# Kernel tuning notes

Measured on AMD Instinct MI355X. Metric: run time of the kernel, lower is better.

The kernel has to match this reference:

```python
import jax, jax.numpy as jnp
import numpy as np

D_H = 768
HEAD = 12
D_ATTN = D_H // HEAD


def setup_inputs() -> dict:
    key = jax.random.key(0)
    ks = jax.random.split(key, 9)
    bz, slen = 2, 4096
    scale = 1.0 / np.sqrt(D_H)
    return {
        "v": jax.random.normal(ks[0], (bz, slen, D_H), jnp.float32),
        "k": jax.random.normal(ks[1], (bz, slen, D_H), jnp.float32),
        "q": jax.random.normal(ks[2], (bz, slen, D_H), jnp.float32),
        "mask": jax.random.randint(ks[3], (bz, 1, 1, slen), 0, 2, jnp.int32),
        "w_v": jax.random.normal(ks[4], (D_H, D_H), jnp.float32) * scale,
        "w_k": jax.random.normal(ks[5], (D_H, D_H), jnp.float32) * scale,
        "w_q": jax.random.normal(ks[6], (D_H, D_H), jnp.float32) * scale,
        "w_o": jax.random.normal(ks[7], (D_H, D_H), jnp.float32) * scale,
        "b_o": jax.random.normal(ks[8], (D_H,), jnp.float32) * 0.02,
    }


def _split_head(x, seq_len):
    # (bz, len, d_h) -> (bz, head, len, d_attn)
    bz = x.shape[0]
    return x.reshape(bz, seq_len, HEAD, D_ATTN).transpose(0, 2, 1, 3)


def reference(v, k, q, mask, w_v, w_k, w_q, w_o, b_o):
    len_k, len_q = k.shape[1], q.shape[1]
    vh = _split_head(v @ w_v, len_k)   # (bz, head, len_k, d_attn)
    kh = _split_head(k @ w_k, len_k)
    qh = _split_head(q @ w_q, len_q)
    # scaled dot-product attention with additive mask
    weight = jnp.einsum("bhqd,bhkd->bhqk", qh, kh) / jnp.sqrt(
        jnp.asarray(D_ATTN, jnp.float32)
    )
    weight = weight + mask.astype(weight.dtype) * (-1e9)
    scale_weight = jax.nn.softmax(weight, axis=-1)
    attn = jnp.einsum("bhqk,bhkd->bhqd", scale_weight, vh)
    attn = attn.transpose(0, 2, 1, 3).reshape(-1, len_q, D_H)
    return attn @ w_o + b_o
```

## Files before the change

### kernel.cpp

```cpp
#include <hip/hip_runtime.h>
#include <hip/hip_bf16.h>

#define SLEN 4096
#define DH 768
#define NHEAD 12
#define DA 64

using short8 = __attribute__((ext_vector_type(8))) short;
using f32x4  = __attribute__((ext_vector_type(4))) float;
typedef unsigned uv2 __attribute__((ext_vector_type(2)));

static __device__ __forceinline__ unsigned short f2b(float f) {
    union { __hip_bfloat16 h; unsigned short u; } c;
    c.h = __float2bfloat16(f);
    return c.u;
}

static __device__ __forceinline__ unsigned pkbf(float a, float b) {
    __hip_bfloat162 h = __float22bfloat162_rn(float2{a, b});
    union { __hip_bfloat162 h; unsigned u; } c; c.h = h; return c.u;
}

static __device__ __forceinline__ float fexp2(float x) {
    float r; asm("v_exp_f32 %0, %1" : "=v"(r) : "v"(x)); return r;
}

static __device__ __forceinline__ void swap32(unsigned& a, unsigned& b, int g1) {
#if __has_builtin(__builtin_amdgcn_permlane32_swap)
    uv2 r = __builtin_amdgcn_permlane32_swap(a, b, false, false);
    a = r.x; b = r.y;
#else
    unsigned own = g1 ? b : a, send = g1 ? a : b;
    unsigned recv = __shfl_xor(send, 32);
    unsigned nlo = g1 ? recv : own;
    unsigned nhi = g1 ? own : recv;
    a = nlo; b = nhi;
#endif
}

static __device__ __forceinline__ void swap16(unsigned& a, unsigned& b, int g0) {
#if __has_builtin(__builtin_amdgcn_permlane16_swap)
    uv2 r = __builtin_amdgcn_permlane16_swap(a, b, false, false);
    a = r.x; b = r.y;
#else
    unsigned own = g0 ? b : a, send = g0 ? a : b;
    unsigned recv = __shfl_xor(send, 16);
    unsigned nlo = g0 ? recv : own;
    unsigned nhi = g0 ? own : recv;
    a = nlo; b = nhi;
#endif
}

#define GLD_LDS16(gp, lp) __builtin_amdgcn_global_load_lds( \
    (const __attribute__((address_space(1))) unsigned int*)(gp), \
    (__attribute__((address_space(3))) unsigned int*)(lp), 16, 0, 0)

#define CSCALE 0.18033688011f
#define BIASSTRIDE 4352

__global__ __launch_bounds__(256) void wtrans4(const float* __restrict__ w_v, const float* __restrict__ w_k,
                                               const float* __restrict__ w_q, const float* __restrict__ w_o,
                                               unsigned short* __restrict__ WtV, unsigned short* __restrict__ WtK,
                                               unsigned short* __restrict__ WtQ, unsigned short* __restrict__ WtO,
                                               const int* __restrict__ mask, int* __restrict__ idx,
                                               float* __restrict__ biasC, int* __restrict__ nktArr) {
    const int z = blockIdx.y;
    const int t = threadIdx.x;
    if (z == 4) {
        if (blockIdx.x >= 2) return;
        __shared__ int psum[256];
        const int b = blockIdx.x;
        const int s0 = t * 16;
        const int* mb = mask + b * SLEN;
        int keep[16]; int cnt = 0;
#pragma unroll
        for (int j = 0; j < 16; ++j) { keep[j] = (mb[s0 + j] == 0); cnt += keep[j]; }
        psum[t] = cnt;
        __syncthreads();
        for (int off = 1; off < 256; off <<= 1) {
            int v = psum[t];
            int u = (t >= off) ? psum[t - off] : 0;
            __syncthreads();
            psum[t] = v + u;
            __syncthreads();
        }
        int excl = psum[t] - cnt;
        int total = psum[255];
        int* ib = idx + b * SLEN;
#pragma unroll
        for (int j = 0; j < 16; ++j)
            if (keep[j]) ib[excl++] = s0 + j;
        for (int j = total + t; j < SLEN; j += 256) ib[j] = 0;
        int nkt = (total + 63) >> 6;
        if (nkt < 2) nkt = 2;
        if (t == 0) { nktArr[b] = nkt; nktArr[2 + b] = total; }
        float* bb = biasC + b * BIASSTRIDE;
        for (int j = t; j < BIASSTRIDE; j += 256) bb[j] = (j < total) ? 0.f : -1.442695041e9f;
        return;
    }
    const float* W = (z == 0) ? w_v : (z == 1) ? w_k : (z == 2) ? w_q : w_o;
    unsigned short* Wt = (z == 0) ? WtV : (z == 1) ? WtK : (z == 2) ? WtQ : WtO;
    __shared__ float tile[64][65];
    const int tk = blockIdx.x / 12, tn = blockIdx.x % 12;
    const int k0 = tk * 64, n0 = tn * 64;
#pragma unroll
    for (int i = 0; i < 4; ++i) {
        int uid = t + 256 * i;
        int r = uid >> 4, c = (uid & 15) * 4;
        float4 v4 = *reinterpret_cast<const float4*>(W + (size_t)(k0 + r) * DH + n0 + c);
        tile[r][c] = v4.x; tile[r][c + 1] = v4.y; tile[r][c + 2] = v4.z; tile[r][c + 3] = v4.w;
    }
    __syncthreads();
#pragma unroll
    for (int i = 0; i < 2; ++i) {
        int uid = t + 256 * i;
        int n = uid >> 3, c = (uid & 7) * 8;
        union { unsigned short us[8]; uint4 u; } pk;
#pragma unroll
        for (int j = 0; j < 8; ++j) pk.us[j] = f2b(tile[c + j][n]);
        *reinterpret_cast<uint4*>(Wt + (size_t)(n0 + n) * DH + k0 + c) = pk.u;
    }
}

__global__ __launch_bounds__(256, 3) void proj3(const float* __restrict__ vin, const float* __restrict__ kin,
                                                const float* __restrict__ qin,
                                                const unsigned short* __restrict__ WtV,
                                                const unsigned short* __restrict__ WtK,
                                                const unsigned short* __restrict__ WtQ,
                                                unsigned short* __restrict__ VhTc,
                                                unsigned short* __restrict__ Khc,
                                                unsigned short* __restrict__ Qh,
                                                const int* __restrict__ idx,
                                                const int* __restrict__ nktArr) {
    __shared__ __align__(16) char smem[49152];
    const int t = threadIdx.x;
    const int w = t >> 6, lane = t & 63, lr = lane & 15, lg = lane >> 4;
    const int zz = blockIdx.y;
    const int z = zz / 6, panel = zz % 6;
    const float* X = (z == 0) ? vin : (z == 1) ? kin : qin;
    const unsigned short* Wt = (z == 0) ? WtV : (z == 1) ? WtK : WtQ;
    const int b = blockIdx.x >> 5;
    const int r128 = (blockIdx.x & 31) * 128;
    const bool gather = (z != 2);
    if (gather && r128 >= nktArr[b] * 64) return;
    const int n0 = panel * 128;

    const float* ap[4];
#pragma unroll
    for (int g = 0; g < 4; ++g) {
        int row = w * 32 + g * 8 + (lane >> 3);
        int grow = b * SLEN + (gather ? idx[b * SLEN + r128 + row] : (r128 + row));
        int cj = (lane & 7) ^ (row & 7);
        ap[g] = X + (size_t)grow * DH + cj * 4;
    }
    const unsigned short* bp2[2];
#pragma unroll
    for (int g = 0; g < 2; ++g) {
        int n = w * 32 + g * 16 + (lane >> 2);
        int cj = (lane & 3) ^ (n & 3);
        bp2[g] = Wt + (size_t)(n0 + n) * DH + cj * 8;
    }

    const int arow = w * 32 + lr;
    const int lr7 = lr & 7, lr3 = lr & 3;

    f32x4 acc[2][8] = {};

#define STAGE(PAR) do {                                                              \
        char* ab_ = smem + (PAR) * 16384 + w * 4096;                                 \
        char* bb_ = smem + 32768 + (PAR) * 8192 + w * 2048;                          \
        GLD_LDS16(ap[0], ab_);         GLD_LDS16(ap[1], ab_ + 1024);                 \
        GLD_LDS16(ap[2], ab_ + 2048);  GLD_LDS16(ap[3], ab_ + 3072);                 \
        GLD_LDS16(bp2[0], bb_);        GLD_LDS16(bp2[1], bb_ + 1024);                \
        ap[0] += 32; ap[1] += 32; ap[2] += 32; ap[3] += 32;                          \
        bp2[0] += 32; bp2[1] += 32;                                                  \
    } while (0)

    STAGE(0);
    __syncthreads();

    for (int kt = 0; kt < 24; ++kt) {
        const int par = kt & 1;
        if (kt < 23) STAGE(par ^ 1);
        const char* bufA = smem + par * 16384;
        const char* bufB = smem + 32768 + par * 8192;
        short8 af[2];
#pragma unroll
        for (int mi = 0; mi < 2; ++mi) {
            int r = arow + mi * 16;
            f32x4 alo = *reinterpret_cast<const f32x4*>(bufA + r * 128 + ((2 * lg) ^ lr7) * 16);
            f32x4 ahi = *reinterpret_cast<const f32x4*>(bufA + r * 128 + ((2 * lg + 1) ^ lr7) * 16);
            union { unsigned u[4]; short8 s; } pk;
            pk.u[0] = pkbf(alo[0], alo[1]);
            pk.u[1] = pkbf(alo[2], alo[3]);
            pk.u[2] = pkbf(ahi[0], ahi[1]);
            pk.u[3] = pkbf(ahi[2], ahi[3]);
            af[mi] = pk.s;
        }
        __builtin_amdgcn_s_setprio(1);
#pragma unroll
        for (int ni = 0; ni < 8; ++ni) {
            int n = ni * 16 + lr;
            short8 bf = *reinterpret_cast<const short8*>(bufB + n * 64 + (lg ^ lr3) * 16);
            acc[0][ni] = __builtin_amdgcn_mfma_f32_16x16x32_bf16(af[0], bf, acc[0][ni], 0, 0, 0);
            acc[1][ni] = __builtin_amdgcn_mfma_f32_16x16x32_bf16(af[1], bf, acc[1][ni], 0, 0, 0);
        }
        __builtin_amdgcn_s_setprio(0);
        __syncthreads();
    }
#undef STAGE

    if (z == 0) {
        unsigned short (*tile)[136] = reinterpret_cast<unsigned short(*)[136]>(smem);
#pragma unroll
        for (int mi = 0; mi < 2; ++mi)
#pragma unroll
            for (int ni = 0; ni < 8; ++ni) {
                int n = ni * 16 + lr;
                int j = w * 32 + mi * 16 + lg * 4;
                *reinterpret_cast<unsigned*>(&tile[n][j])     = pkbf(acc[mi][ni][0], acc[mi][ni][1]);
                *reinterpret_cast<unsigned*>(&tile[n][j + 2]) = pkbf(acc[mi][ni][2], acc[mi][ni][3]);
            }
        __syncthreads();
        int n = t >> 1, jc = (t & 1) * 64;
        unsigned short* dst = VhTc +
            ((size_t)(b * NHEAD + 2 * panel + (n >> 6)) * DA + (n & 63)) * SLEN + r128 + jc;
#pragma unroll
        for (int c = 0; c < 8; ++c)
            *reinterpret_cast<uint4*>(dst + c * 8) = *reinterpret_cast<const uint4*>(&tile[n][jc + c * 8]);
    } else {
        unsigned short* Y = (z == 1) ? Khc : Qh;
        const float scale = (z == 2) ? CSCALE : 1.0f;
#pragma unroll
        for (int mi = 0; mi < 2; ++mi)
#pragma unroll
            for (int ni = 0; ni < 8; ++ni) {
                int n = n0 + ni * 16 + lr;
                int h = n >> 6, d = n & 63;
#pragma unroll
                for (int r = 0; r < 4; ++r) {
                    int s = r128 + w * 32 + mi * 16 + lg * 4 + r;
                    Y[(size_t)((b * NHEAD + h) * SLEN + s) * DA + d] = f2b(acc[mi][ni][r] * scale);
                }
            }
    }
}

__global__ __launch_bounds__(256, 3) void attn_kernel(const unsigned short* __restrict__ Qh,
                                                      const unsigned short* __restrict__ Kh,
                                                      const unsigned short* __restrict__ VhT,
                                                      const float* __restrict__ biasC,
                                                      const int* __restrict__ nktArr,
                                                      unsigned short* __restrict__ AT) {
    __shared__ __align__(16) char smem[49152];
    const int t = threadIdx.x;
    const int w = t >> 6, lane = t & 63, lr = lane & 15, lg = lane >> 4;
    const int g0 = (lane >> 4) & 1, g1 = (lane >> 5) & 1;
    const int lr7 = lr & 7;

    const int i = blockIdx.x;
    const int bh = (i & 7) * 3 + ((i >> 3) >> 5);
    const int qb = (i >> 3) & 31;
    const int b = bh / NHEAD;
    const int q0 = qb * 128;
    const size_t base = (size_t)bh * SLEN * DA;
    const int wq0 = q0 + w * 32;
    const int nkt = nktArr[b];
    const int padStart = nktArr[2 + b] >> 6;

    short8 qf[2][2];
#pragma unroll
    for (int mi = 0; mi < 2; ++mi)
#pragma unroll
        for (int ks = 0; ks < 2; ++ks)
            qf[mi][ks] = *reinterpret_cast<const short8*>(
                Qh + base + (size_t)(wq0 + mi * 16 + lr) * DA + ks * 32 + lg * 8);

    const int uid0 = (w << 6) | lane;
    const int r0 = uid0 >> 3;
    const int sc0 = ((uid0 & 7) ^ (r0 & 7)) * 8;
    const unsigned short* kp = Kh + base + (size_t)r0 * DA + sc0;
    const unsigned short* vp = VhT + ((size_t)bh * DA + r0) * SLEN + sc0;
    const float* biasB = biasC + b * BIASSTRIDE + lg * 4;

    const int a0 = lr * 128 + ((lg) ^ lr7) * 16;
    const int a1 = lr * 128 + ((4 + lg) ^ lr7) * 16;

    f32x4 st[2][4];
    f32x4 oacc[2][4] = {};
    f32x4 oacc_l[2] = {};
    f32x4 bias_c[4] = {};
    short8 pa[2][2];
    union { unsigned u[4]; short8 s; } ones;
    ones.u[0] = 0x3F803F80u; ones.u[1] = 0x3F803F80u; ones.u[2] = 0x3F803F80u; ones.u[3] = 0x3F803F80u;

#define STAGE(CB) do {                                                   \
        GLD_LDS16(kp,              smem + (CB) + w * 1024);              \
        GLD_LDS16(kp + 2048,       smem + (CB) + (4 + w) * 1024);        \
        GLD_LDS16(vp,              smem + (CB) + 8192 + w * 1024);       \
        GLD_LDS16(vp + 32 * SLEN,  smem + (CB) + 8192 + (4 + w) * 1024); \
        kp += 64 * DA; vp += 64;                                         \
    } while (0)

#define BIASCOND(TT) do {                                                        \
        if ((TT) >= padStart) {                                                  \
            const float* bpp_ = biasB + (TT) * 64;                               \
            _Pragma("unroll") for (int ni = 0; ni < 4; ++ni)                     \
                bias_c[ni] = *reinterpret_cast<const f32x4*>(bpp_ + ni * 16);    \
        }                                                                        \
    } while (0)

#define QKT(NB) do {                                                                           \
        _Pragma("unroll") for (int ni = 0; ni < 4; ++ni) {                                     \
            short8 kf0 = *reinterpret_cast<const short8*>(smem + (NB) + ni * 2048 + a0);       \
            short8 kf1 = *reinterpret_cast<const short8*>(smem + (NB) + ni * 2048 + a1);       \
            st[0][ni] = __builtin_amdgcn_mfma_f32_16x16x32_bf16(kf1, qf[0][1],                 \
                        __builtin_amdgcn_mfma_f32_16x16x32_bf16(kf0, qf[0][0], bias_c[ni], 0, 0, 0), 0, 0, 0); \
            st[1][ni] = __builtin_amdgcn_mfma_f32_16x16x32_bf16(kf1, qf[1][1],                 \
                        __builtin_amdgcn_mfma_f32_16x16x32_bf16(kf0, qf[1][0], bias_c[ni], 0, 0, 0), 0, 0, 0); \
        }                                                                                      \
    } while (0)

#define PV(CB) do {                                                                                  \
        _Pragma("unroll") for (int ni = 0; ni < 4; ++ni) {                                           \
            short8 vf0 = *reinterpret_cast<const short8*>(smem + (CB) + 8192 + ni * 2048 + a0);      \
            short8 vf1 = *reinterpret_cast<const short8*>(smem + (CB) + 8192 + ni * 2048 + a1);      \
            oacc[0][ni] = __builtin_amdgcn_mfma_f32_16x16x32_bf16(vf0, pa[0][0], oacc[0][ni], 0, 0, 0); \
            oacc[0][ni] = __builtin_amdgcn_mfma_f32_16x16x32_bf16(vf1, pa[0][1], oacc[0][ni], 0, 0, 0); \
            oacc[1][ni] = __builtin_amdgcn_mfma_f32_16x16x32_bf16(vf0, pa[1][0], oacc[1][ni], 0, 0, 0); \
            oacc[1][ni] = __builtin_amdgcn_mfma_f32_16x16x32_bf16(vf1, pa[1][1], oacc[1][ni], 0, 0, 0); \
        }                                                                                            \
        oacc_l[0] = __builtin_amdgcn_mfma_f32_16x16x32_bf16(ones.s, pa[0][0], oacc_l[0], 0, 0, 0);   \
        oacc_l[0] = __builtin_amdgcn_mfma_f32_16x16x32_bf16(ones.s, pa[0][1], oacc_l[0], 0, 0, 0);   \
        oacc_l[1] = __builtin_amdgcn_mfma_f32_16x16x32_bf16(ones.s, pa[1][0], oacc_l[1], 0, 0, 0);   \
        oacc_l[1] = __builtin_amdgcn_mfma_f32_16x16x32_bf16(ones.s, pa[1][1], oacc_l[1], 0, 0, 0);   \
    } while (0)

#define SOFTMAX do {                                                                               \
        _Pragma("unroll") for (int mi = 0; mi < 2; ++mi) {                                         \
            unsigned D[8];                                                                         \
            _Pragma("unroll") for (int ni = 0; ni < 4; ++ni) {                                     \
                float p0 = fexp2(st[mi][ni][0]);                                                   \
                float p1 = fexp2(st[mi][ni][1]);                                                   \
                float p2 = fexp2(st[mi][ni][2]);                                                   \
                float p3 = fexp2(st[mi][ni][3]);                                                   \
                D[ni * 2] = pkbf(p0, p1);                                                          \
                D[ni * 2 + 1] = pkbf(p2, p3);                                                      \
            }                                                                                      \
            swap32(D[0], D[2], g1); swap32(D[1], D[3], g1);                                        \
            swap32(D[4], D[6], g1); swap32(D[5], D[7], g1);                                        \
            swap16(D[0], D[2], g0); swap16(D[1], D[3], g0);                                        \
            swap16(D[4], D[6], g0); swap16(D[5], D[7], g0);                                        \
            union { unsigned u[4]; short8 s; } c0, c1;                                             \
            c0.u[0] = D[0]; c0.u[1] = D[1]; c0.u[2] = D[2]; c0.u[3] = D[3];                        \
            c1.u[0] = D[4]; c1.u[1] = D[5]; c1.u[2] = D[6]; c1.u[3] = D[7];                        \
            pa[mi][0] = c0.s; pa[mi][1] = c1.s;                                                    \
        }                                                                                          \
    } while (0)

#define BODY(KT, CB, NB, NNB) do {                                       \
        SOFTMAX;                                                         \
        __syncthreads();                                                 \
        if ((KT) < nkt - 2) STAGE(NNB);                                  \
        BIASCOND((KT) + 1);                                              \
        __builtin_amdgcn_s_setprio(1);                                   \
        QKT(NB);                                                         \
        PV(CB);                                                          \
        __builtin_amdgcn_s_setprio(0);                                   \
    } while (0)

    STAGE(0);
    __syncthreads();
    STAGE(16384);
    BIASCOND(0);
    __builtin_amdgcn_s_setprio(1);
    QKT(0);
    __builtin_amdgcn_s_setprio(0);

    int kt = 0;
    while (kt + 3 <= nkt - 1) {
        BODY(kt,     0,     16384, 32768);
        BODY(kt + 1, 16384, 32768, 0);
        BODY(kt + 2, 32768, 0,     16384);
        kt += 3;
    }
    const int rem = (nkt - 1) - kt;
    if (rem >= 1) BODY(kt,     0,     16384, 32768);
    if (rem >= 2) BODY(kt + 1, 16384, 32768, 0);
    SOFTMAX;
    {
        const int cbF = ((nkt - 1) % 3) * 16384;
        __builtin_amdgcn_s_setprio(1);
        PV(cbF);
        __builtin_amdgcn_s_setprio(0);
    }

#undef BODY
#undef SOFTMAX
#undef PV
#undef QKT
#undef BIASCOND
#undef STAGE

    {
        __syncthreads();
        float inv[2];
        inv[0] = 1.0f / oacc_l[0][0];
        inv[1] = 1.0f / oacc_l[1][0];
        unsigned* Obw = reinterpret_cast<unsigned*>(smem) + w * (32 * 36);
#pragma unroll
        for (int mi = 0; mi < 2; ++mi)
#pragma unroll
            for (int ni = 0; ni < 4; ++ni) {
                uint2 pr;
                pr.x = pkbf(oacc[mi][ni][0] * inv[mi], oacc[mi][ni][1] * inv[mi]);
                pr.y = pkbf(oacc[mi][ni][2] * inv[mi], oacc[mi][ni][3] * inv[mi]);
                *reinterpret_cast<uint2*>(&Obw[(mi * 16 + lr) * 36 + ni * 8 + lg * 2]) = pr;
            }
        __syncthreads();
        int row = lane >> 1, half = lane & 1;
        int qg = q0 + w * 32 + row;
        unsigned short* dst = AT + (size_t)(b * SLEN + qg) * DH + (bh % NHEAD) * DA + half * 32;
#pragma unroll
        for (int c = 0; c < 4; ++c) {
            uint4 v = *reinterpret_cast<const uint4*>(&Obw[row * 36 + half * 16 + c * 4]);
            *reinterpret_cast<uint4*>(dst + c * 8) = v;
        }
    }
}

__global__ __launch_bounds__(256, 3) void proj_out(const unsigned short* __restrict__ X,
                                                   const unsigned short* __restrict__ Wt,
                                                   const float* __restrict__ bias,
                                                   float* __restrict__ Y) {
    __shared__ __align__(16) char smem[49152];
    const int t = threadIdx.x;
    const int w = t >> 6, lane = t & 63, lr = lane & 15, lg = lane >> 4;
    const int row0 = blockIdx.x * 128;
    const int n0 = blockIdx.y * 64;
    const int lr7 = lr & 7;

    const unsigned short* ap[4];
#pragma unroll
    for (int g = 0; g < 4; ++g) {
        int row = w * 32 + g * 8 + (lane >> 3);
        int cj = (lane & 7) ^ (row & 7);
        ap[g] = X + (size_t)(row0 + row) * DH + cj * 8;
    }
    const unsigned short* bp2[2];
#pragma unroll
    for (int g = 0; g < 2; ++g) {
        int n = w * 16 + g * 8 + (lane >> 3);
        int cj = (lane & 7) ^ (n & 7);
        bp2[g] = Wt + (size_t)(n0 + n) * DH + cj * 8;
    }

    f32x4 acc[2][4] = {};

#define STAGE_O(PAR) do {                                                            \
        char* ab_ = smem + (PAR) * 16384 + w * 4096;                                 \
        char* bb_ = smem + 32768 + (PAR) * 8192 + w * 2048;                          \
        GLD_LDS16(ap[0], ab_);         GLD_LDS16(ap[1], ab_ + 1024);                 \
        GLD_LDS16(ap[2], ab_ + 2048);  GLD_LDS16(ap[3], ab_ + 3072);                 \
        GLD_LDS16(bp2[0], bb_);        GLD_LDS16(bp2[1], bb_ + 1024);                \
        ap[0] += 64; ap[1] += 64; ap[2] += 64; ap[3] += 64;                          \
        bp2[0] += 64; bp2[1] += 64;                                                  \
    } while (0)

    STAGE_O(0);
    __syncthreads();

    for (int kt = 0; kt < 12; ++kt) {
        const int par = kt & 1;
        if (kt < 11) STAGE_O(par ^ 1);
        const char* bufA = smem + par * 16384;
        const char* bufB = smem + 32768 + par * 8192;
        short8 af[2][2], bf[4][2];
#pragma unroll
        for (int mi = 0; mi < 2; ++mi) {
            int r = w * 32 + mi * 16 + lr;
#pragma unroll
            for (int ks = 0; ks < 2; ++ks)
                af[mi][ks] = *reinterpret_cast<const short8*>(bufA + r * 128 + ((ks * 4 + lg) ^ lr7) * 16);
        }
#pragma unroll
        for (int ni = 0; ni < 4; ++ni) {
            int n = ni * 16 + lr;
#pragma unroll
            for (int ks = 0; ks < 2; ++ks)
                bf[ni][ks] = *reinterpret_cast<const short8*>(bufB + n * 128 + ((ks * 4 + lg) ^ lr7) * 16);
        }
        __builtin_amdgcn_s_setprio(1);
#pragma unroll
        for (int mi = 0; mi < 2; ++mi)
#pragma unroll
            for (int ni = 0; ni < 4; ++ni) {
                acc[mi][ni] = __builtin_amdgcn_mfma_f32_16x16x32_bf16(af[mi][0], bf[ni][0], acc[mi][ni], 0, 0, 0);
                acc[mi][ni] = __builtin_amdgcn_mfma_f32_16x16x32_bf16(af[mi][1], bf[ni][1], acc[mi][ni], 0, 0, 0);
            }
        __builtin_amdgcn_s_setprio(0);
        __syncthreads();
    }
#undef STAGE_O

#pragma unroll
    for (int ni = 0; ni < 4; ++ni) {
        float bv = bias[n0 + ni * 16 + lr];
#pragma unroll
        for (int mi = 0; mi < 2; ++mi)
#pragma unroll
            for (int r = 0; r < 4; ++r) {
                int row = row0 + w * 32 + mi * 16 + lg * 4 + r;
                Y[(size_t)row * DH + n0 + ni * 16 + lr] = acc[mi][ni][r] + bv;
            }
    }
}

extern "C" void kernel_launch(void* const* d_in, const int* in_sizes, int n_in,
                              void* d_out, int out_size, void* d_ws, size_t ws_size,
                              hipStream_t stream) {
    const float* v   = (const float*)d_in[0];
    const float* k   = (const float*)d_in[1];
    const float* q   = (const float*)d_in[2];
    const int*  mask = (const int*)d_in[3];
    const float* w_v = (const float*)d_in[4];
    const float* w_k = (const float*)d_in[5];
    const float* w_q = (const float*)d_in[6];
    const float* w_o = (const float*)d_in[7];
    const float* b_o = (const float*)d_in[8];
    float* out = (float*)d_out;

    char* ws = (char*)d_ws;
    unsigned short* Qh   = (unsigned short*)(ws);
    unsigned short* Khc  = (unsigned short*)(ws + 12582912);
    unsigned short* AT   = (unsigned short*)(ws + 25165824);
    unsigned short* VhTc = (unsigned short*)(ws + 37748736);
    unsigned short* WtV  = (unsigned short*)(ws + 50331648);
    unsigned short* WtK  = WtV + 589824;
    unsigned short* WtQ  = WtK + 589824;
    unsigned short* WtO  = WtQ + 589824;
    float* biasC = (float*)(ws + 55050240);
    int*   idxA  = (int*)(ws + 55085056);
    int*   nktA  = (int*)(ws + 55117824);

    wtrans4<<<dim3(144, 5), 256, 0, stream>>>(w_v, w_k, w_q, w_o, WtV, WtK, WtQ, WtO,
                                              mask, idxA, biasC, nktA);
    proj3<<<dim3(64, 18), 256, 0, stream>>>(v, k, q, WtV, WtK, WtQ, VhTc, Khc, Qh, idxA, nktA);
    attn_kernel<<<768, 256, 0, stream>>>(Qh, Khc, VhTc, biasC, nktA, AT);
    proj_out<<<dim3(64, 12), 256, 0, stream>>>(AT, WtO, b_o, out);
}
```

Measured before the change: 131.7 us.

## Load K fragments directly into registers instead of staging through LDS

K tiles are no longer copied into shared memory. Each lane loads its MFMA K fragments straight from global memory into two alternating register sets, and only V is staged in LDS. This halves the LDS footprint to 24KB and removes the LDS reads for K. In exchange it raises register pressure and exposes global load latency, since each K tile is loaded only one iteration ahead, and the loop is unrolled to six iterations to keep the register-set parity fixed.

```diff
diff --git a/kernel.cpp b/kernel.cpp
--- a/kernel.cpp
+++ b/kernel.cpp
@@ -252,7 +252,7 @@
                                                       const float* __restrict__ biasC,
                                                       const int* __restrict__ nktArr,
                                                       unsigned short* __restrict__ AT) {
-    __shared__ __align__(16) char smem[49152];
+    __shared__ __align__(16) char smem[24576];
     const int t = threadIdx.x;
     const int w = t >> 6, lane = t & 63, lr = lane & 15, lg = lane >> 4;
     const int g0 = (lane >> 4) & 1, g1 = (lane >> 5) & 1;
@@ -279,8 +279,8 @@
     const int uid0 = (w << 6) | lane;
     const int r0 = uid0 >> 3;
     const int sc0 = ((uid0 & 7) ^ (r0 & 7)) * 8;
-    const unsigned short* kp = Kh + base + (size_t)r0 * DA + sc0;
     const unsigned short* vp = VhT + ((size_t)bh * DA + r0) * SLEN + sc0;
+    const unsigned short* kq = Kh + base + (size_t)lr * DA + lg * 8;
     const float* biasB = biasC + b * BIASSTRIDE + lg * 4;
 
     const int a0 = lr * 128 + ((lg) ^ lr7) * 16;
@@ -291,15 +291,22 @@
     f32x4 oacc_l[2] = {};
     f32x4 bias_c[4] = {};
     short8 pa[2][2];
+    short8 kfA[4][2], kfB[4][2];
     union { unsigned u[4]; short8 s; } ones;
     ones.u[0] = 0x3F803F80u; ones.u[1] = 0x3F803F80u; ones.u[2] = 0x3F803F80u; ones.u[3] = 0x3F803F80u;
 
-#define STAGE(CB) do {                                                   \
-        GLD_LDS16(kp,              smem + (CB) + w * 1024);              \
-        GLD_LDS16(kp + 2048,       smem + (CB) + (4 + w) * 1024);        \
-        GLD_LDS16(vp,              smem + (CB) + 8192 + w * 1024);       \
-        GLD_LDS16(vp + 32 * SLEN,  smem + (CB) + 8192 + (4 + w) * 1024); \
-        kp += 64 * DA; vp += 64;                                         \
+#define STAGE_V(CB) do {                                                 \
+        GLD_LDS16(vp,              smem + (CB) + w * 1024);              \
+        GLD_LDS16(vp + 32 * SLEN,  smem + (CB) + (4 + w) * 1024);        \
+        vp += 64;                                                        \
+    } while (0)
+
+#define KLOAD(SET) do {                                                          \
+        _Pragma("unroll") for (int ni = 0; ni < 4; ++ni) {                       \
+            SET[ni][0] = *reinterpret_cast<const short8*>(kq + ni * 1024);       \
+            SET[ni][1] = *reinterpret_cast<const short8*>(kq + ni * 1024 + 32);  \
+        }                                                                        \
+        kq += 64 * DA;                                                           \
     } while (0)
 
 #define BIASCOND(TT) do {                                                        \
@@ -310,21 +317,19 @@
         }                                                                        \
     } while (0)
 
-#define QKT(NB) do {                                                                           \
+#define QKT(SET) do {                                                                          \
         _Pragma("unroll") for (int ni = 0; ni < 4; ++ni) {                                     \
-            short8 kf0 = *reinterpret_cast<const short8*>(smem + (NB) + ni * 2048 + a0);       \
-            short8 kf1 = *reinterpret_cast<const short8*>(smem + (NB) + ni * 2048 + a1);       \
-            st[0][ni] = __builtin_amdgcn_mfma_f32_16x16x32_bf16(kf1, qf[0][1],                 \
-                        __builtin_amdgcn_mfma_f32_16x16x32_bf16(kf0, qf[0][0], bias_c[ni], 0, 0, 0), 0, 0, 0); \
-            st[1][ni] = __builtin_amdgcn_mfma_f32_16x16x32_bf16(kf1, qf[1][1],                 \
-                        __builtin_amdgcn_mfma_f32_16x16x32_bf16(kf0, qf[1][0], bias_c[ni], 0, 0, 0), 0, 0, 0); \
+            st[0][ni] = __builtin_amdgcn_mfma_f32_16x16x32_bf16(SET[ni][1], qf[0][1],          \
+                        __builtin_amdgcn_mfma_f32_16x16x32_bf16(SET[ni][0], qf[0][0], bias_c[ni], 0, 0, 0), 0, 0, 0); \
+            st[1][ni] = __builtin_amdgcn_mfma_f32_16x16x32_bf16(SET[ni][1], qf[1][1],          \
+                        __builtin_amdgcn_mfma_f32_16x16x32_bf16(SET[ni][0], qf[1][0], bias_c[ni], 0, 0, 0), 0, 0, 0); \
         }                                                                                      \
     } while (0)
 
 #define PV(CB) do {                                                                                  \
         _Pragma("unroll") for (int ni = 0; ni < 4; ++ni) {                                           \
-            short8 vf0 = *reinterpret_cast<const short8*>(smem + (CB) + 8192 + ni * 2048 + a0);      \
-            short8 vf1 = *reinterpret_cast<const short8*>(smem + (CB) + 8192 + ni * 2048 + a1);      \
+            short8 vf0 = *reinterpret_cast<const short8*>(smem + (CB) + ni * 2048 + a0);             \
+            short8 vf1 = *reinterpret_cast<const short8*>(smem + (CB) + ni * 2048 + a1);             \
             oacc[0][ni] = __builtin_amdgcn_mfma_f32_16x16x32_bf16(vf0, pa[0][0], oacc[0][ni], 0, 0, 0); \
             oacc[0][ni] = __builtin_amdgcn_mfma_f32_16x16x32_bf16(vf1, pa[0][1], oacc[0][ni], 0, 0, 0); \
             oacc[1][ni] = __builtin_amdgcn_mfma_f32_16x16x32_bf16(vf0, pa[1][0], oacc[1][ni], 0, 0, 0); \
@@ -358,38 +363,46 @@
         }                                                                                          \
     } while (0)
 
-#define BODY(KT, CB, NB, NNB) do {                                       \
+#define BODY(KT, CB, NNB, CURSET, NXTSET) do {                           \
         SOFTMAX;                                                         \
         __syncthreads();                                                 \
-        if ((KT) < nkt - 2) STAGE(NNB);                                  \
+        if ((KT) < nkt - 2) { STAGE_V(NNB); KLOAD(NXTSET); }             \
         BIASCOND((KT) + 1);                                              \
         __builtin_amdgcn_s_setprio(1);                                   \
-        QKT(NB);                                                         \
+        QKT(CURSET);                                                     \
         PV(CB);                                                          \
         __builtin_amdgcn_s_setprio(0);                                   \
     } while (0)
 
-    STAGE(0);
+    STAGE_V(0);
+    KLOAD(kfA);
     __syncthreads();
-    STAGE(16384);
+    STAGE_V(8192);
+    KLOAD(kfB);
     BIASCOND(0);
     __builtin_amdgcn_s_setprio(1);
-    QKT(0);
+    QKT(kfA);
     __builtin_amdgcn_s_setprio(0);
 
     int kt = 0;
-    while (kt + 3 <= nkt - 1) {
-        BODY(kt,     0,     16384, 32768);
-        BODY(kt + 1, 16384, 32768, 0);
-        BODY(kt + 2, 32768, 0,     16384);
-        kt += 3;
+    while (kt + 6 <= nkt - 1) {
+        BODY(kt + 0, 0,     16384, kfB, kfA);
+        BODY(kt + 1, 8192,  0,     kfA, kfB);
+        BODY(kt + 2, 16384, 8192,  kfB, kfA);
+        BODY(kt + 3, 0,     16384, kfA, kfB);
+        BODY(kt + 4, 8192,  0,     kfB, kfA);
+        BODY(kt + 5, 16384, 8192,  kfA, kfB);
+        kt += 6;
     }
     const int rem = (nkt - 1) - kt;
-    if (rem >= 1) BODY(kt,     0,     16384, 32768);
-    if (rem >= 2) BODY(kt + 1, 16384, 32768, 0);
+    if (rem >= 1) BODY(kt + 0, 0,     16384, kfB, kfA);
+    if (rem >= 2) BODY(kt + 1, 8192,  0,     kfA, kfB);
+    if (rem >= 3) BODY(kt + 2, 16384, 8192,  kfB, kfA);
+    if (rem >= 4) BODY(kt + 3, 0,     16384, kfA, kfB);
+    if (rem >= 5) BODY(kt + 4, 8192,  0,     kfB, kfA);
     SOFTMAX;
     {
-        const int cbF = ((nkt - 1) % 3) * 16384;
+        const int cbF = ((nkt - 1) % 3) * 8192;
         __builtin_amdgcn_s_setprio(1);
         PV(cbF);
         __builtin_amdgcn_s_setprio(0);
@@ -400,7 +413,8 @@
 #undef PV
 #undef QKT
 #undef BIASCOND
-#undef STAGE
+#undef KLOAD
+#undef STAGE_V
 
     {
         __syncthreads();
```

Result: slower. 359.9 us (+173.4%).
